# Kernel optimization log

Hardware: AMD Instinct MI355X
Metric: run time of the kernel (lower is better)

Reference implementation:

```python
import jax, jax.numpy as jnp
import numpy as np

N_NODES = 50000
N_EDGES = 800000
IN_DIM = 128
HID = 128
OUT_DIM = 2


def setup_inputs() -> dict:
    key = jax.random.key(0)
    ks = jax.random.split(key, 10)
    s_in = 1.0 / np.sqrt(IN_DIM)
    s_cat = 1.0 / np.sqrt(2 * HID)
    s_h = 1.0 / np.sqrt(HID)
    return {
        "x": jax.random.normal(ks[0], (N_NODES, IN_DIM), dtype=jnp.float32),
        "edge_index": jax.random.randint(ks[1], (2, N_EDGES), 0, N_NODES, dtype=jnp.int64),
        "W_in": jax.random.uniform(ks[2], (IN_DIM, HID), jnp.float32, -s_in, s_in),
        "b_in": jnp.zeros((HID,), jnp.float32),
        "W1": jax.random.uniform(ks[3], (2 * HID, HID), jnp.float32, -s_cat, s_cat),
        "b1": jnp.zeros((HID,), jnp.float32),
        "W2": jax.random.uniform(ks[4], (HID, HID), jnp.float32, -s_h, s_h),
        "b2": jnp.zeros((HID,), jnp.float32),
        "Wc": jax.random.uniform(ks[5], (HID, OUT_DIM), jnp.float32, -s_h, s_h),
        "bc": jnp.zeros((OUT_DIM,), jnp.float32),
    }


def reference(x, edge_index, W_in, b_in, W1, b1, W2, b2, Wc, bc):
    # Input projection (eval mode: dropout is identity)
    h = jax.nn.relu(x @ W_in + b_in)                      # [N, H]
    src, dst = edge_index[0], edge_index[1]               # PyG: x_j = x[src], x_i = x[dst]
    # Per-edge message: MLP(h_i || h_j). Split the first Linear over the concat
    # halves to avoid materializing the [E, 2H] concat buffer.
    m = h[dst] @ W1[:HID] + h[src] @ W1[HID:] + b1        # [E, H]
    m = jax.nn.relu(m) @ W2 + b2                          # [E, H]
    # Scatter-add aggregation into destination nodes
    h2 = jax.ops.segment_sum(m, dst, num_segments=N_NODES)  # [N, H]
    h2 = jax.nn.relu(h2)
    return h2 @ Wc + bc                                   # [N, OUT]
```

## Files before the change

### kernel.cpp

```cpp
#include <hip/hip_runtime.h>
#include <hip/hip_bf16.h>

#define N_NODES 50000
#define N_EDGES 800000
#define HID 128
#define NPROJ 391
#define NPERM 3125
#define CAP 48
#define OVF_MAX 8192

typedef __bf16 bf16x8 __attribute__((ext_vector_type(8)));
typedef float f32x4 __attribute__((ext_vector_type(4)));

__global__ __launch_bounds__(256) void prep_kernel(
    const float* __restrict__ Win, const float* __restrict__ W1,
    const float* __restrict__ W2, __bf16* __restrict__ Wsw)
{
    int id = blockIdx.x * 256 + threadIdx.x;
    int m     = id >> 14;
    int rem   = id & 16383;
    int j     = rem & 7;
    int lane  = (rem >> 3) & 63;
    int ntile = (rem >> 9) & 7;
    int kstep = rem >> 12;
    int k = kstep * 32 + (lane >> 4) * 8 + j;
    int n = ntile * 16 + (lane & 15);
    float v;
    if (m == 0)      v = Win[k * HID + n];
    else if (m == 1) v = W1[k * HID + n];
    else if (m == 2) v = W1[(k + HID) * HID + n];
    else             v = W2[k * HID + n];
    Wsw[id] = (__bf16)v;
}

__global__ __launch_bounds__(256) void mega_kernel(
    const float* __restrict__ x, const __bf16* __restrict__ Wsw,
    const float* __restrict__ b_in, const float* __restrict__ b1,
    float* __restrict__ P1a, __bf16* __restrict__ P1b,
    const int* __restrict__ eidx, int* __restrict__ cursor,
    unsigned short* __restrict__ srt, int* __restrict__ ovf_cnt,
    uint2* __restrict__ ovf)
{
    int bb = blockIdx.x;
    int tid = threadIdx.x;

    if (bb >= NPROJ) {
        int e = (bb - NPROJ) * 256 + tid;
        if (e < N_EDGES) {
            int d = eidx[N_EDGES + e];
            int s = eidx[e];
            int p = atomicAdd(&cursor[d], 1);
            if (p < CAP) {
                srt[d * CAP + p] = (unsigned short)s;
            } else {
                int o = atomicAdd(ovf_cnt, 1);
                if (o < OVF_MAX) ovf[o] = make_uint2((unsigned)d, (unsigned)s);
            }
        }
        return;
    }

    __shared__ __bf16 At[128][136];
    int wave = tid >> 6, lane = tid & 63;
    int r_lane = lane & 15, quad = lane >> 4;
    int m0 = bb * 128;

    for (int i = tid; i < 128 * 32; i += 256) {
        int r = i >> 5, c = i & 31;
        int row = m0 + r;
        float4 v = make_float4(0.f, 0.f, 0.f, 0.f);
        if (row < N_NODES) v = *(const float4*)(x + (long)row * HID + c * 4);
        __bf16* dst = &At[r][c * 4];
        dst[0] = (__bf16)v.x; dst[1] = (__bf16)v.y;
        dst[2] = (__bf16)v.z; dst[3] = (__bf16)v.w;
    }
    __syncthreads();

    {
        f32x4 acc[2][8] = {};
#pragma unroll
        for (int ks = 0; ks < 4; ++ks) {
            int kb = ks * 32 + quad * 8;
            bf16x8 a0 = *(const bf16x8*)(&At[wave * 32 + r_lane][kb]);
            bf16x8 a1 = *(const bf16x8*)(&At[wave * 32 + 16 + r_lane][kb]);
#pragma unroll
            for (int n = 0; n < 8; ++n) {
                bf16x8 b = *(const bf16x8*)(Wsw + ((ks * 8 + n) * 64 + lane) * 8);
                acc[0][n] = __builtin_amdgcn_mfma_f32_16x16x32_bf16(a0, b, acc[0][n], 0, 0, 0);
                acc[1][n] = __builtin_amdgcn_mfma_f32_16x16x32_bf16(a1, b, acc[1][n], 0, 0, 0);
            }
        }
#pragma unroll
        for (int n = 0; n < 8; ++n) {
            int col = n * 16 + r_lane;
            float bias = b_in[col];
#pragma unroll
            for (int mt = 0; mt < 2; ++mt) {
                int rb = wave * 32 + mt * 16 + quad * 4;
#pragma unroll
                for (int r = 0; r < 4; ++r) {
                    float v = acc[mt][n][r] + bias;
                    At[rb + r][col] = (__bf16)(v > 0.f ? v : 0.f);
                }
            }
        }
    }
    __syncthreads();

    {
        const __bf16* W1a = Wsw + 16384;
        f32x4 acc[2][8] = {};
#pragma unroll
        for (int ks = 0; ks < 4; ++ks) {
            int kb = ks * 32 + quad * 8;
            bf16x8 a0 = *(const bf16x8*)(&At[wave * 32 + r_lane][kb]);
            bf16x8 a1 = *(const bf16x8*)(&At[wave * 32 + 16 + r_lane][kb]);
#pragma unroll
            for (int n = 0; n < 8; ++n) {
                bf16x8 b = *(const bf16x8*)(W1a + ((ks * 8 + n) * 64 + lane) * 8);
                acc[0][n] = __builtin_amdgcn_mfma_f32_16x16x32_bf16(a0, b, acc[0][n], 0, 0, 0);
                acc[1][n] = __builtin_amdgcn_mfma_f32_16x16x32_bf16(a1, b, acc[1][n], 0, 0, 0);
            }
        }
#pragma unroll
        for (int n = 0; n < 8; ++n) {
            int col = n * 16 + r_lane;
            float bias = b1[col];
#pragma unroll
            for (int mt = 0; mt < 2; ++mt) {
                int rbase = m0 + wave * 32 + mt * 16 + quad * 4;
#pragma unroll
                for (int r = 0; r < 4; ++r) {
                    int row = rbase + r;
                    if (row < N_NODES)
                        P1a[(long)row * HID + col] = acc[mt][n][r] + bias;
                }
            }
        }
    }

    {
        const __bf16* W1b = Wsw + 32768;
        f32x4 acc[2][8] = {};
#pragma unroll
        for (int ks = 0; ks < 4; ++ks) {
            int kb = ks * 32 + quad * 8;
            bf16x8 a0 = *(const bf16x8*)(&At[wave * 32 + r_lane][kb]);
            bf16x8 a1 = *(const bf16x8*)(&At[wave * 32 + 16 + r_lane][kb]);
#pragma unroll
            for (int n = 0; n < 8; ++n) {
                bf16x8 b = *(const bf16x8*)(W1b + ((ks * 8 + n) * 64 + lane) * 8);
                acc[0][n] = __builtin_amdgcn_mfma_f32_16x16x32_bf16(a0, b, acc[0][n], 0, 0, 0);
                acc[1][n] = __builtin_amdgcn_mfma_f32_16x16x32_bf16(a1, b, acc[1][n], 0, 0, 0);
            }
        }
#pragma unroll
        for (int n = 0; n < 8; ++n) {
            int col = n * 16 + r_lane;
#pragma unroll
            for (int mt = 0; mt < 2; ++mt) {
                int rbase = m0 + wave * 32 + mt * 16 + quad * 4;
#pragma unroll
                for (int r = 0; r < 4; ++r) {
                    int row = rbase + r;
                    if (row < N_NODES)
                        P1b[(long)row * HID + col] = (__bf16)acc[mt][n][r];
                }
            }
        }
    }
}

__device__ inline void acc8(float4& rA, float4& rB,
                            const float4 paA, const float4 paB, uint4 q)
{
    float t;
    t = paA.x + __uint_as_float(q.x << 16);         rA.x += t > 0.f ? t : 0.f;
    t = paA.y + __uint_as_float(q.x & 0xffff0000u); rA.y += t > 0.f ? t : 0.f;
    t = paA.z + __uint_as_float(q.y << 16);         rA.z += t > 0.f ? t : 0.f;
    t = paA.w + __uint_as_float(q.y & 0xffff0000u); rA.w += t > 0.f ? t : 0.f;
    t = paB.x + __uint_as_float(q.z << 16);         rB.x += t > 0.f ? t : 0.f;
    t = paB.y + __uint_as_float(q.z & 0xffff0000u); rB.y += t > 0.f ? t : 0.f;
    t = paB.z + __uint_as_float(q.w << 16);         rB.z += t > 0.f ? t : 0.f;
    t = paB.w + __uint_as_float(q.w & 0xffff0000u); rB.w += t > 0.f ? t : 0.f;
}

__global__ __launch_bounds__(512) void aggnode_kernel(
    const float* __restrict__ P1a, const __bf16* __restrict__ P1b,
    const unsigned short* __restrict__ srt, const int* __restrict__ cursor,
    const int* __restrict__ ovf_cnt, const uint2* __restrict__ ovf,
    const __bf16* __restrict__ Wsw, const float* __restrict__ b2,
    const float* __restrict__ Wc, const float* __restrict__ bc,
    float* __restrict__ out)
{
    __shared__ __bf16 At[128][136];
    int tid = threadIdx.x;
    int m0 = blockIdx.x * 128;
    int oc = *ovf_cnt;
    if (oc > OVF_MAX) oc = OVF_MAX;

    {
        int team = tid >> 4;
        int tl = tid & 15;
        for (int g = 0; g < 4; ++g) {
            int r = team * 4 + g;
            int node = m0 + r;
            float4 rA = make_float4(0.f, 0.f, 0.f, 0.f);
            float4 rB = make_float4(0.f, 0.f, 0.f, 0.f);
            if (node < N_NODES) {
                int beg = node * CAP;
                int degT = cursor[node];
                int deg = degT > CAP ? CAP : degT;
                const float* par = P1a + (long)node * HID + tl * 8;
                float4 paA = *(const float4*)par;
                float4 paB = *(const float4*)(par + 4);
                int j = 0;
                for (; j + 8 <= deg; j += 8) {
                    int s0 = srt[beg + j];
                    int s1 = srt[beg + j + 1];
                    int s2 = srt[beg + j + 2];
                    int s3 = srt[beg + j + 3];
                    int s4 = srt[beg + j + 4];
                    int s5 = srt[beg + j + 5];
                    int s6 = srt[beg + j + 6];
                    int s7 = srt[beg + j + 7];
                    uint4 q0 = *(const uint4*)(P1b + (long)s0 * HID + tl * 8);
                    uint4 q1 = *(const uint4*)(P1b + (long)s1 * HID + tl * 8);
                    uint4 q2 = *(const uint4*)(P1b + (long)s2 * HID + tl * 8);
                    uint4 q3 = *(const uint4*)(P1b + (long)s3 * HID + tl * 8);
                    uint4 q4 = *(const uint4*)(P1b + (long)s4 * HID + tl * 8);
                    uint4 q5 = *(const uint4*)(P1b + (long)s5 * HID + tl * 8);
                    uint4 q6 = *(const uint4*)(P1b + (long)s6 * HID + tl * 8);
                    uint4 q7 = *(const uint4*)(P1b + (long)s7 * HID + tl * 8);
                    acc8(rA, rB, paA, paB, q0);
                    acc8(rA, rB, paA, paB, q1);
                    acc8(rA, rB, paA, paB, q2);
                    acc8(rA, rB, paA, paB, q3);
                    acc8(rA, rB, paA, paB, q4);
                    acc8(rA, rB, paA, paB, q5);
                    acc8(rA, rB, paA, paB, q6);
                    acc8(rA, rB, paA, paB, q7);
                }
                for (; j < deg; ++j) {
                    int s = srt[beg + j];
                    uint4 q = *(const uint4*)(P1b + (long)s * HID + tl * 8);
                    acc8(rA, rB, paA, paB, q);
                }
                if (oc) {
                    for (int t = 0; t < oc; ++t) {
                        uint2 e = ovf[t];
                        if ((int)e.x == node) {
                            uint4 q = *(const uint4*)(P1b + (long)e.y * HID + tl * 8);
                            acc8(rA, rB, paA, paB, q);
                        }
                    }
                }
            }
            __bf16 vv[8];
            vv[0] = (__bf16)rA.x; vv[1] = (__bf16)rA.y;
            vv[2] = (__bf16)rA.z; vv[3] = (__bf16)rA.w;
            vv[4] = (__bf16)rB.x; vv[5] = (__bf16)rB.y;
            vv[6] = (__bf16)rB.z; vv[7] = (__bf16)rB.w;
            *(uint4*)(&At[r][tl * 8]) = *(uint4*)vv;
        }
    }
    __syncthreads();

    int wave = tid >> 6, lane = tid & 63;
    int r_lane = lane & 15, quad = lane >> 4;
    const __bf16* W2f = Wsw + 49152;
    f32x4 acc[8] = {};
#pragma unroll
    for (int ks = 0; ks < 4; ++ks) {
        int kb = ks * 32 + quad * 8;
        bf16x8 a0 = *(const bf16x8*)(&At[wave * 16 + r_lane][kb]);
#pragma unroll
        for (int n = 0; n < 8; ++n) {
            bf16x8 b = *(const bf16x8*)(W2f + ((ks * 8 + n) * 64 + lane) * 8);
            acc[n] = __builtin_amdgcn_mfma_f32_16x16x32_bf16(a0, b, acc[n], 0, 0, 0);
        }
    }

#pragma unroll
    for (int r = 0; r < 4; ++r) {
        int row = m0 + wave * 16 + quad * 4 + r;
        float deg = (row < N_NODES) ? (float)cursor[row] : 0.f;
        float s0 = 0.f, s1 = 0.f;
#pragma unroll
        for (int n = 0; n < 8; ++n) {
            int col = n * 16 + r_lane;
            float v = acc[n][r] + deg * b2[col];
            v = v > 0.f ? v : 0.f;
            s0 += v * Wc[col * 2 + 0];
            s1 += v * Wc[col * 2 + 1];
        }
#pragma unroll
        for (int off = 1; off < 16; off <<= 1) {
            s0 += __shfl_xor(s0, off);
            s1 += __shfl_xor(s1, off);
        }
        if (r_lane == 0 && row < N_NODES) {
            out[(long)row * 2 + 0] = s0 + bc[0];
            out[(long)row * 2 + 1] = s1 + bc[1];
        }
    }
}

extern "C" void kernel_launch(void* const* d_in, const int* in_sizes, int n_in,
                              void* d_out, int out_size, void* d_ws, size_t ws_size,
                              hipStream_t stream) {
    const float* x    = (const float*)d_in[0];
    const int* eidx   = (const int*)d_in[1];
    const float* W_in = (const float*)d_in[2];
    const float* b_in = (const float*)d_in[3];
    const float* W1   = (const float*)d_in[4];
    const float* b1   = (const float*)d_in[5];
    const float* W2   = (const float*)d_in[6];
    const float* b2   = (const float*)d_in[7];
    const float* Wc   = (const float*)d_in[8];
    const float* bc   = (const float*)d_in[9];
    float* out = (float*)d_out;

    char* ws = (char*)d_ws;
    float*  P1a  = (float*)(ws + 0);
    __bf16* P1b  = (__bf16*)(ws + 25600000);
    unsigned short* srt = (unsigned short*)(ws + 38400000);
    int* cursor  = (int*)(ws + 43200000);
    int* ovf_cnt = (int*)(ws + 43400000);
    uint2* ovf   = (uint2*)(ws + 43400064);
    __bf16* Wsw  = (__bf16*)(ws + 43465600);

    hipMemsetAsync(cursor, 0, 200064, stream);

    prep_kernel<<<256, 256, 0, stream>>>(W_in, W1, W2, Wsw);
    mega_kernel<<<NPROJ + NPERM, 256, 0, stream>>>(x, Wsw, b_in, b1, P1a, P1b,
                                                   eidx, cursor, srt, ovf_cnt, ovf);
    aggnode_kernel<<<(N_NODES + 127) / 128, 512, 0, stream>>>(
        P1a, P1b, srt, cursor, ovf_cnt, ovf, Wsw, b2, Wc, bc, out);
}
```

Before: 184.5 us.

## Split per-node edge buckets into four groups to reduce atomic contention

Edges are bucketed into four sub-buckets per destination node, chosen by block index, each holding up to 16 slots. This spreads the atomic cursor increments across more addresses. The aggregation kernel walks all four sub-buckets, stores the summed degree in shared memory for the bias term, and the separate memset is folded into the prep kernel as a zeroing loop. In exchange the aggregation loop has more short, partly unrolled segments, and the srt and cursor footprints grow. The overflow path now triggers when any one group of a node exceeds 16 edges rather than when the node exceeds 48.

Result: slower. 217.6 us (+18.0%).

```diff
diff --git a/kernel.cpp b/kernel.cpp
--- a/kernel.cpp
+++ b/kernel.cpp
@@ -6,7 +6,8 @@
 #define HID 128
 #define NPROJ 391
 #define NPERM 3125
-#define CAP 48
+#define GROUPS 4
+#define CAPX 16
 #define OVF_MAX 8192
 
 typedef __bf16 bf16x8 __attribute__((ext_vector_type(8)));
@@ -14,7 +15,8 @@
 
 __global__ __launch_bounds__(256) void prep_kernel(
     const float* __restrict__ Win, const float* __restrict__ W1,
-    const float* __restrict__ W2, __bf16* __restrict__ Wsw)
+    const float* __restrict__ W2, __bf16* __restrict__ Wsw,
+    int* __restrict__ curz)
 {
     int id = blockIdx.x * 256 + threadIdx.x;
     int m     = id >> 14;
@@ -31,6 +33,7 @@
     else if (m == 2) v = W1[(k + HID) * HID + n];
     else             v = W2[k * HID + n];
     Wsw[id] = (__bf16)v;
+    for (int i = id; i < GROUPS * N_NODES + 16; i += 65536) curz[i] = 0;
 }
 
 __global__ __launch_bounds__(256) void mega_kernel(
@@ -49,9 +52,10 @@
         if (e < N_EDGES) {
             int d = eidx[N_EDGES + e];
             int s = eidx[e];
-            int p = atomicAdd(&cursor[d], 1);
-            if (p < CAP) {
-                srt[d * CAP + p] = (unsigned short)s;
+            int slot = (bb & (GROUPS - 1)) * N_NODES + d;
+            int p = atomicAdd(&cursor[slot], 1);
+            if (p < CAPX) {
+                srt[slot * CAPX + p] = (unsigned short)s;
             } else {
                 int o = atomicAdd(ovf_cnt, 1);
                 if (o < OVF_MAX) ovf[o] = make_uint2((unsigned)d, (unsigned)s);
@@ -194,6 +198,7 @@
     float* __restrict__ out)
 {
     __shared__ __bf16 At[128][136];
+    __shared__ int degS[128];
     int tid = threadIdx.x;
     int m0 = blockIdx.x * 128;
     int oc = *ovf_cnt;
@@ -207,44 +212,50 @@
             int node = m0 + r;
             float4 rA = make_float4(0.f, 0.f, 0.f, 0.f);
             float4 rB = make_float4(0.f, 0.f, 0.f, 0.f);
+            int degsum = 0;
             if (node < N_NODES) {
-                int beg = node * CAP;
-                int degT = cursor[node];
-                int deg = degT > CAP ? CAP : degT;
                 const float* par = P1a + (long)node * HID + tl * 8;
                 float4 paA = *(const float4*)par;
                 float4 paB = *(const float4*)(par + 4);
-                int j = 0;
-                for (; j + 8 <= deg; j += 8) {
-                    int s0 = srt[beg + j];
-                    int s1 = srt[beg + j + 1];
-                    int s2 = srt[beg + j + 2];
-                    int s3 = srt[beg + j + 3];
-                    int s4 = srt[beg + j + 4];
-                    int s5 = srt[beg + j + 5];
-                    int s6 = srt[beg + j + 6];
-                    int s7 = srt[beg + j + 7];
-                    uint4 q0 = *(const uint4*)(P1b + (long)s0 * HID + tl * 8);
-                    uint4 q1 = *(const uint4*)(P1b + (long)s1 * HID + tl * 8);
-                    uint4 q2 = *(const uint4*)(P1b + (long)s2 * HID + tl * 8);
-                    uint4 q3 = *(const uint4*)(P1b + (long)s3 * HID + tl * 8);
-                    uint4 q4 = *(const uint4*)(P1b + (long)s4 * HID + tl * 8);
-                    uint4 q5 = *(const uint4*)(P1b + (long)s5 * HID + tl * 8);
-                    uint4 q6 = *(const uint4*)(P1b + (long)s6 * HID + tl * 8);
-                    uint4 q7 = *(const uint4*)(P1b + (long)s7 * HID + tl * 8);
-                    acc8(rA, rB, paA, paB, q0);
-                    acc8(rA, rB, paA, paB, q1);
-                    acc8(rA, rB, paA, paB, q2);
-                    acc8(rA, rB, paA, paB, q3);
-                    acc8(rA, rB, paA, paB, q4);
-                    acc8(rA, rB, paA, paB, q5);
-                    acc8(rA, rB, paA, paB, q6);
-                    acc8(rA, rB, paA, paB, q7);
-                }
-                for (; j < deg; ++j) {
-                    int s = srt[beg + j];
-                    uint4 q = *(const uint4*)(P1b + (long)s * HID + tl * 8);
-                    acc8(rA, rB, paA, paB, q);
+#pragma unroll
+                for (int gq = 0; gq < GROUPS; ++gq) {
+                    int slot = gq * N_NODES + node;
+                    int dT = cursor[slot];
+                    degsum += dT;
+                    int deg = dT > CAPX ? CAPX : dT;
+                    int beg = slot * CAPX;
+                    int j = 0;
+                    for (; j + 8 <= deg; j += 8) {
+                        int s0 = srt[beg + j];
+                        int s1 = srt[beg + j + 1];
+                        int s2 = srt[beg + j + 2];
+                        int s3 = srt[beg + j + 3];
+                        int s4 = srt[beg + j + 4];
+                        int s5 = srt[beg + j + 5];
+                        int s6 = srt[beg + j + 6];
+                        int s7 = srt[beg + j + 7];
+                        uint4 q0 = *(const uint4*)(P1b + (long)s0 * HID + tl * 8);
+                        uint4 q1 = *(const uint4*)(P1b + (long)s1 * HID + tl * 8);
+                        uint4 q2 = *(const uint4*)(P1b + (long)s2 * HID + tl * 8);
+                        uint4 q3 = *(const uint4*)(P1b + (long)s3 * HID + tl * 8);
+                        uint4 q4 = *(const uint4*)(P1b + (long)s4 * HID + tl * 8);
+                        uint4 q5 = *(const uint4*)(P1b + (long)s5 * HID + tl * 8);
+                        uint4 q6 = *(const uint4*)(P1b + (long)s6 * HID + tl * 8);
+                        uint4 q7 = *(const uint4*)(P1b + (long)s7 * HID + tl * 8);
+                        acc8(rA, rB, paA, paB, q0);
+                        acc8(rA, rB, paA, paB, q1);
+                        acc8(rA, rB, paA, paB, q2);
+                        acc8(rA, rB, paA, paB, q3);
+                        acc8(rA, rB, paA, paB, q4);
+                        acc8(rA, rB, paA, paB, q5);
+                        acc8(rA, rB, paA, paB, q6);
+                        acc8(rA, rB, paA, paB, q7);
+                    }
+                    for (; j < deg; ++j) {
+                        int s = srt[beg + j];
+                        uint4 q = *(const uint4*)(P1b + (long)s * HID + tl * 8);
+                        acc8(rA, rB, paA, paB, q);
+                    }
                 }
                 if (oc) {
                     for (int t = 0; t < oc; ++t) {
@@ -256,6 +267,7 @@
                     }
                 }
             }
+            if (tl == 0) degS[r] = degsum;
             __bf16 vv[8];
             vv[0] = (__bf16)rA.x; vv[1] = (__bf16)rA.y;
             vv[2] = (__bf16)rA.z; vv[3] = (__bf16)rA.w;
@@ -283,8 +295,9 @@
 
 #pragma unroll
     for (int r = 0; r < 4; ++r) {
-        int row = m0 + wave * 16 + quad * 4 + r;
-        float deg = (row < N_NODES) ? (float)cursor[row] : 0.f;
+        int lr = wave * 16 + quad * 4 + r;
+        int row = m0 + lr;
+        float deg = (float)degS[lr];
         float s0 = 0.f, s1 = 0.f;
 #pragma unroll
         for (int n = 0; n < 8; ++n) {
@@ -325,14 +338,12 @@
     float*  P1a  = (float*)(ws + 0);
     __bf16* P1b  = (__bf16*)(ws + 25600000);
     unsigned short* srt = (unsigned short*)(ws + 38400000);
-    int* cursor  = (int*)(ws + 43200000);
-    int* ovf_cnt = (int*)(ws + 43400000);
-    uint2* ovf   = (uint2*)(ws + 43400064);
-    __bf16* Wsw  = (__bf16*)(ws + 43465600);
-
-    hipMemsetAsync(cursor, 0, 200064, stream);
-
-    prep_kernel<<<256, 256, 0, stream>>>(W_in, W1, W2, Wsw);
+    int* cursor  = (int*)(ws + 44800000);
+    int* ovf_cnt = (int*)(ws + 45600000);
+    uint2* ovf   = (uint2*)(ws + 45600064);
+    __bf16* Wsw  = (__bf16*)(ws + 45665600);
+
+    prep_kernel<<<256, 256, 0, stream>>>(W_in, W1, W2, Wsw, cursor);
     mega_kernel<<<NPROJ + NPERM, 256, 0, stream>>>(x, Wsw, b_in, b1, P1a, P1b,
                                                    eidx, cursor, srt, ovf_cnt, ovf);
     aggnode_kernel<<<(N_NODES + 127) / 128, 512, 0, stream>>>(
```
